# Kernel tuning notes

Measured on AMD Instinct MI355X. Metric: run time of the kernel, lower is better.

The kernel has to match this reference:

```python
import jax, jax.numpy as jnp
import numpy as np

B, N, C, H = 64, 577, 768, 12
D = C // H
SCALE = D ** -0.5


def setup_inputs() -> dict:
    key = jax.random.key(0)
    ks = jax.random.split(key, 5)
    s = 0.02
    return {
        "x": jax.random.normal(ks[0], (B, N, C), dtype=jnp.float32),
        "qkv_w": jax.random.normal(ks[1], (3 * C, C), dtype=jnp.float32) * s,
        "qkv_b": jax.random.normal(ks[2], (3 * C,), dtype=jnp.float32) * s,
        "proj_w": jax.random.normal(ks[3], (C, C), dtype=jnp.float32) * s,
        "proj_b": jax.random.normal(ks[4], (C,), dtype=jnp.float32) * s,
    }


def reference(x, qkv_w, qkv_b, proj_w, proj_b):
    b, n, c = x.shape
    # Full QKV projection (as in the original module): [B,N,3C] -> [B,N,3,H,D]
    qkv = (x @ qkv_w.T + qkv_b).reshape(b, n, 3, H, D)
    qc = qkv[:, :1, 0]   # class-token query only: [B,1,H,D]
    k = qkv[:, :, 1]     # [B,N,H,D]
    v = qkv[:, :, 2]     # [B,N,H,D]
    # single-query attention scores per head: [B,H,N]
    attn = jnp.einsum("bohd,bnhd->bhn", qc, k) * SCALE
    attn = jax.nn.softmax(attn, axis=-1)
    # weighted sum of values -> [B,H,D] -> [B,1,C]
    cls = jnp.einsum("bhn,bnhd->bhd", attn, v).reshape(b, 1, c)
    cls = cls @ proj_w.T + proj_b
    return jnp.concatenate([cls, x[:, 1:]], axis=1)
```

## Files before the change

kernel.cpp:

```cpp
#include <hip/hip_runtime.h>

#define Bz 64
#define Nn 577
#define Cc 768
#define Hh 12
#define Dd 64
#define SCALE 0.125f
#define YSEG 8

typedef __attribute__((ext_vector_type(8))) short short8;
typedef __attribute__((ext_vector_type(4))) float float4v;

__device__ __forceinline__ unsigned short bf16rne(float f) {
  unsigned u = __float_as_uint(f);
  u += 0x7FFFu + ((u >> 16) & 1u);
  return (unsigned short)(u >> 16);
}

__device__ __forceinline__ short8 cvt8(float4 a, float4 b) {
  short8 v;
  v[0] = (short)bf16rne(a.x); v[1] = (short)bf16rne(a.y);
  v[2] = (short)bf16rne(a.z); v[3] = (short)bf16rne(a.w);
  v[4] = (short)bf16rne(b.x); v[5] = (short)bf16rne(b.y);
  v[6] = (short)bf16rne(b.z); v[7] = (short)bf16rne(b.w);
  return v;
}

__device__ __forceinline__ short8 cvt8v(float4v a, float4v b) {
  short8 v;
  v[0] = (short)bf16rne(a[0]); v[1] = (short)bf16rne(a[1]);
  v[2] = (short)bf16rne(a[2]); v[3] = (short)bf16rne(a[3]);
  v[4] = (short)bf16rne(b[0]); v[5] = (short)bf16rne(b[1]);
  v[6] = (short)bf16rne(b[2]); v[7] = (short)bf16rne(b[3]);
  return v;
}


template <int MODE, int SEGS>
__global__ __launch_bounds__(256) void k_gemm64(const float* __restrict__ A,
                                                const float* __restrict__ W,
                                                const float* __restrict__ bias,
                                                float* __restrict__ out) {
  int tile = blockIdx.x;
  int jt = tile % 48, bt = tile / 48;
  int wave = threadIdx.x >> 6, lane = threadIdx.x & 63;
  int m = lane & 15, quad = lane >> 4;
  int brow = bt * 16 + m;
  int jrow = jt * 16 + m;
  size_t aoff;
  if (MODE == 0)      aoff = (size_t)brow * (Nn * Cc);
  else if (MODE == 1) aoff = (size_t)brow * (SEGS * Hh * Cc) + (size_t)(jt >> 2) * Cc;
  else                aoff = (size_t)brow * Cc;
  size_t woff = (MODE == 1) ? (size_t)(2 * Cc + jrow) * Cc : (size_t)jrow * Cc;
  const float4v* Ap = (const float4v*)(A + aoff) + wave * 48 + quad * 2;
  const float4v* Wp = (const float4v*)(W + woff) + wave * 48 + quad * 2;
  float4v acc = {0.f, 0.f, 0.f, 0.f};
#pragma unroll
  for (int s = 0; s < 6; ++s) {
    float4v a0, a1;
    if (MODE == 1 && SEGS > 1) {
      a0 = (float4v){0.f, 0.f, 0.f, 0.f};
      a1 = a0;
#pragma unroll
      for (int seg = 0; seg < SEGS; ++seg) {
        a0 += Ap[seg * 2304 + s * 8];
        a1 += Ap[seg * 2304 + s * 8 + 1];
      }
    } else {
      a0 = Ap[s * 8]; a1 = Ap[s * 8 + 1];
    }
    float4v w0 = Wp[s * 8], w1 = Wp[s * 8 + 1];
    acc = __builtin_amdgcn_mfma_f32_16x16x32_bf16(cvt8v(a0, a1), cvt8v(w0, w1),
                                                  acc, 0, 0, 0);
  }
  __shared__ float red[4][64][4];
#pragma unroll
  for (int reg = 0; reg < 4; ++reg) red[wave][lane][reg] = acc[reg];
  __syncthreads();
  if (wave == 0) {
#pragma unroll
    for (int reg = 0; reg < 4; ++reg) {
      float v = red[0][lane][reg] + red[1][lane][reg] +
                red[2][lane][reg] + red[3][lane][reg];
      int j = jt * 16 + m;
      int bb = bt * 16 + quad * 4 + reg;
      float bv = (MODE == 1) ? bias[2 * Cc + j] : bias[j];
      if (MODE == 2) out[(size_t)bb * (Nn * Cc) + j] = v + bv;
      else           out[(size_t)bb * Cc + j] = v + bv;
    }
  }
}

__global__ __launch_bounds__(256) void k_r(const float* __restrict__ qf,
                                           const float* __restrict__ qkv_w,
                                           unsigned short* __restrict__ rb) {
  int h = blockIdx.x % Hh, bg = blockIdx.x / Hh;
  int t = threadIdx.x;
  __shared__ float qs2[Dd][4];
  {
    int bb = t >> 6, d = t & 63;
    qs2[d][bb] = qf[(size_t)(bg * 4 + bb) * Cc + h * Dd + d];
  }
  __syncthreads();
  float acc[4][3];
#pragma unroll
  for (int bb = 0; bb < 4; ++bb)
#pragma unroll
    for (int i = 0; i < 3; ++i) acc[bb][i] = 0.f;
  const float* wk = qkv_w + (size_t)(Cc + h * Dd) * Cc;
  for (int d = 0; d < Dd; ++d) {
    float w0 = wk[(size_t)d * Cc + t];
    float w1 = wk[(size_t)d * Cc + t + 256];
    float w2 = wk[(size_t)d * Cc + t + 512];
    float4 qa = *(const float4*)&qs2[d][0];
    float qv[4] = {qa.x, qa.y, qa.z, qa.w};
#pragma unroll
    for (int bb = 0; bb < 4; ++bb) {
      acc[bb][0] += qv[bb] * w0;
      acc[bb][1] += qv[bb] * w1;
      acc[bb][2] += qv[bb] * w2;
    }
  }
#pragma unroll
  for (int bb = 0; bb < 4; ++bb) {
    size_t base = (size_t)(bg * 4 + bb) * 12288 + h * 8;
#pragma unroll
    for (int i = 0; i < 3; ++i) {
      int c = t + i * 256;
      int s = c >> 5, qq = (c >> 3) & 3, j = c & 7;
      rb[base + s * 512 + qq * 128 + j] = bf16rne(acc[bb][i] * SCALE);
    }
  }
}

__global__ __launch_bounds__(512) void k_logits(const float* __restrict__ x,
                                                const unsigned short* __restrict__ rb,
                                                float* __restrict__ logits) {
  int b = blockIdx.x / 10, tile = blockIdx.x % 10;
  int wave = threadIdx.x >> 6, lane = threadIdx.x & 63;
  int g = wave & 3, kh = wave >> 2;
  int m = lane & 15, quad = lane >> 4;
  int n = tile * 64 + g * 16 + m;
  int nc = n > 576 ? 576 : n;
  const short8* ag = (const short8*)(rb + (size_t)b * 12288);
  const float4* xg = (const float4*)(x + (size_t)b * Nn * Cc) + (size_t)nc * 192 + quad * 2;
  float4v acc = {0.f, 0.f, 0.f, 0.f};
#pragma unroll
  for (int i = 0; i < 12; ++i) {
    int s = kh * 12 + i;
    short8 a = ag[s * 64 + quad * 16 + m];
    float4 f0 = xg[s * 8], f1 = xg[s * 8 + 1];
    acc = __builtin_amdgcn_mfma_f32_16x16x32_bf16(a, cvt8(f0, f1), acc, 0, 0, 0);
  }
  __shared__ float red[4][64][4];
  if (kh == 1) {
#pragma unroll
    for (int reg = 0; reg < 4; ++reg) red[g][lane][reg] = acc[reg];
  }
  __syncthreads();
  if (kh == 0 && n < Nn) {
#pragma unroll
    for (int reg = 0; reg < 4; ++reg) {
      int hh = quad * 4 + reg;
      if (hh < Hh)
        logits[((size_t)b * Hh + hh) * Nn + n] = acc[reg] + red[g][lane][reg];
    }
  }
}

__global__ __launch_bounds__(64) void k_softmax(const float* __restrict__ logits,
                                                float* __restrict__ attnT) {
  int bh = blockIdx.x;
  int b = bh / Hh, h = bh % Hh;
  const float* row = logits + (size_t)bh * Nn;
  int t = threadIdx.x;
  float vals[10];
  float m = -1e30f;
#pragma unroll
  for (int i = 0; i < 10; ++i) {
    int n = i * 64 + t;
    vals[i] = (n < Nn) ? row[n] : -1e30f;
    m = fmaxf(m, vals[i]);
  }
#pragma unroll
  for (int off = 32; off; off >>= 1) m = fmaxf(m, __shfl_down(m, off));
  m = __shfl(m, 0);
  float s = 0.f;
#pragma unroll
  for (int i = 0; i < 10; ++i) { vals[i] = __expf(vals[i] - m); s += vals[i]; }
#pragma unroll
  for (int off = 32; off; off >>= 1) s += __shfl_down(s, off);
  float inv = 1.f / __shfl(s, 0);
#pragma unroll
  for (int i = 0; i < 10; ++i) {
    int n = i * 64 + t;
    if (n < Nn) attnT[((size_t)b * Nn + n) * Hh + h] = vals[i] * inv;
  }
}

__global__ __launch_bounds__(576) void k_y3c(const float* __restrict__ x,
                                             const float* __restrict__ attnT,
                                             float* __restrict__ ypart,
                                             float* __restrict__ out) {
  int b = blockIdx.x / YSEG, seg = blockIdx.x % YSEG;
  int c4 = threadIdx.x % 192;
  int sub = threadIdx.x / 192;
  int n0 = seg * Nn / YSEG, n1 = (seg + 1) * Nn / YSEG;
  int len = n1 - n0;
  int a0 = n0 + sub * len / 3, a1 = n0 + (sub + 1) * len / 3;
  float4v acc[Hh];
#pragma unroll
  for (int h = 0; h < Hh; ++h) acc[h] = (float4v){0.f, 0.f, 0.f, 0.f};
  const float4v* x4 = (const float4v*)(x + (size_t)b * Nn * Cc);
  float4v* o4 = (float4v*)(out + (size_t)b * Nn * Cc);
  const float* at = attnT + (size_t)b * Nn * Hh;
#pragma unroll 8
  for (int n = a0; n < a1; ++n) {
    float4v xv = x4[(size_t)n * 192 + c4];
    if (n)
      __builtin_nontemporal_store(xv, o4 + (size_t)n * 192 + c4);
#pragma unroll
    for (int h = 0; h < Hh; ++h) acc[h] += at[n * Hh + h] * xv;
  }
  __shared__ float4v red[192][Hh];
  if (sub == 2) {
#pragma unroll
    for (int h = 0; h < Hh; ++h) red[c4][h] = acc[h];
  }
  __syncthreads();
  if (sub == 1) {
#pragma unroll
    for (int h = 0; h < Hh; ++h) { acc[h] += red[c4][h]; red[c4][h] = acc[h]; }
  }
  __syncthreads();
  if (sub == 0) {
    float4v* yp = (float4v*)(ypart + ((size_t)(b * YSEG + seg)) * (Hh * Cc));
#pragma unroll
    for (int h = 0; h < Hh; ++h) yp[h * 192 + c4] = acc[h] + red[c4][h];
  }
}

__global__ __launch_bounds__(256) void k_zero(float* __restrict__ y) {
  ((float4*)y)[blockIdx.x * 256 + threadIdx.x] = make_float4(0.f, 0.f, 0.f, 0.f);
}

__global__ __launch_bounds__(192) void k_y_atomic(const float* __restrict__ x,
                                                  const float* __restrict__ attnT,
                                                  float* __restrict__ y) {
  int b = blockIdx.x / YSEG, seg = blockIdx.x % YSEG;
  int n0 = seg * Nn / YSEG, n1 = (seg + 1) * Nn / YSEG;
  int c4 = threadIdx.x;
  float4 acc[Hh];
#pragma unroll
  for (int h = 0; h < Hh; ++h) acc[h] = make_float4(0.f, 0.f, 0.f, 0.f);
  const float4* x4 = (const float4*)(x + (size_t)b * Nn * Cc);
  const float* at = attnT + (size_t)b * Nn * Hh;
#pragma unroll 8
  for (int n = n0; n < n1; ++n) {
    float4 xv = x4[(size_t)n * 192 + c4];
#pragma unroll
    for (int h = 0; h < Hh; ++h) {
      float a = at[n * Hh + h];
      acc[h].x += a * xv.x; acc[h].y += a * xv.y;
      acc[h].z += a * xv.z; acc[h].w += a * xv.w;
    }
  }
  float* yb = y + (size_t)b * Hh * Cc;
#pragma unroll
  for (int h = 0; h < Hh; ++h) {
    float* p = yb + h * Cc + c4 * 4;
    atomicAdd(p + 0, acc[h].x); atomicAdd(p + 1, acc[h].y);
    atomicAdd(p + 2, acc[h].z); atomicAdd(p + 3, acc[h].w);
  }
}

__global__ __launch_bounds__(256) void k_copy(const float* __restrict__ x,
                                              float* __restrict__ out) {
  int idx = blockIdx.x * 256 + threadIdx.x;
  const float4* xi = (const float4*)x;
  float4* oo = (float4*)out;
  for (int i = idx; i < 7077888; i += 262144) {
    int b = i / 110592;
    int r = i - b * 110592;
    size_t off = (size_t)b * 110784 + 192 + r;
    oo[off] = xi[off];
  }
}

extern "C" void kernel_launch(void* const* d_in, const int* in_sizes, int n_in,
                              void* d_out, int out_size, void* d_ws, size_t ws_size,
                              hipStream_t stream) {
  const float* x      = (const float*)d_in[0];
  const float* qkv_w  = (const float*)d_in[1];
  const float* qkv_b  = (const float*)d_in[2];
  const float* proj_w = (const float*)d_in[3];
  const float* proj_b = (const float*)d_in[4];
  float* out = (float*)d_out;
  float* ws = (float*)d_ws;

  unsigned short* rb = (unsigned short*)ws;
  float* qf     = ws + 393216;
  float* logits = ws + 442368;
  float* attnT  = ws + 885504;
  float* ypart  = ws + 1328640;
  float* cls    = ws + 6047232;

  const size_t NEED_PART = (size_t)6096384 * 4;

  if (ws_size >= NEED_PART) {
    k_gemm64<0, 1><<<192, 256, 0, stream>>>(x, qkv_w, qkv_b, qf);
    k_r<<<192, 256, 0, stream>>>(qf, qkv_w, rb);
    k_logits<<<Bz * 10, 512, 0, stream>>>(x, rb, logits);
    k_softmax<<<Bz * Hh, 64, 0, stream>>>(logits, attnT);
    k_y3c<<<Bz * YSEG, 576, 0, stream>>>(x, attnT, ypart, out);
    k_gemm64<1, YSEG><<<192, 256, 0, stream>>>(ypart, qkv_w, qkv_b, cls);
    k_gemm64<2, 1><<<192, 256, 0, stream>>>(cls, proj_w, proj_b, out);
  } else {
    float* y     = ws + 1328640;
    float* cls_c = ws + 1918464;
    k_zero<<<576, 256, 0, stream>>>(y);
    k_gemm64<0, 1><<<192, 256, 0, stream>>>(x, qkv_w, qkv_b, qf);
    k_r<<<192, 256, 0, stream>>>(qf, qkv_w, rb);
    k_logits<<<Bz * 10, 512, 0, stream>>>(x, rb, logits);
    k_softmax<<<Bz * Hh, 64, 0, stream>>>(logits, attnT);
    k_y_atomic<<<Bz * YSEG, 192, 0, stream>>>(x, attnT, y);
    k_gemm64<1, 1><<<192, 256, 0, stream>>>(y, qkv_w, qkv_b, cls_c);
    k_gemm64<2, 1><<<192, 256, 0, stream>>>(cls_c, proj_w, proj_b, out);
  }
}
```

Before: 292.7 us.

## Fuse q projection into k_r and softmax into value-weighted sum kernel

Computes the class-token query projection inside the k-folding kernel, removing the separate q GEMM launch and its workspace round trip. The logits kernel drops the split-K across waves and its shared-memory reduction, so each wave runs the full 24-step reduction. Softmax is folded into the y kernel: each block recomputes per-head max and sum from logits and applies exp on the fly, removing the softmax kernel and the attnT buffer. In exchange, max/sum work is repeated by every segment block and exp is evaluated inside the hot loop, and logits are read with a strided per-head pattern. The fallback path also gains a k_copy launch.

```diff
diff --git a/kernel.cpp b/kernel.cpp
--- a/kernel.cpp
+++ b/kernel.cpp
@@ -91,15 +91,32 @@
   }
 }
 
-__global__ __launch_bounds__(256) void k_r(const float* __restrict__ qf,
-                                           const float* __restrict__ qkv_w,
-                                           unsigned short* __restrict__ rb) {
+__global__ __launch_bounds__(256) void k_rq(const float* __restrict__ x,
+                                            const float* __restrict__ qkv_w,
+                                            const float* __restrict__ qkv_b,
+                                            unsigned short* __restrict__ rb) {
   int h = blockIdx.x % Hh, bg = blockIdx.x / Hh;
   int t = threadIdx.x;
+  __shared__ float x0s[4 * Cc];
   __shared__ float qs2[Dd][4];
   {
-    int bb = t >> 6, d = t & 63;
-    qs2[d][bb] = qf[(size_t)(bg * 4 + bb) * Cc + h * Dd + d];
+    const float4v* xg = (const float4v*)x;
+#pragma unroll
+    for (int k = 0; k < 3; ++k) {
+      int slot = t + k * 256;
+      int bb = slot / 192, c4 = slot % 192;
+      ((float4v*)x0s)[slot] = xg[(size_t)(bg * 4 + bb) * 110784 + c4];
+    }
+  }
+  __syncthreads();
+  {
+    int d = t & 63, bb = t >> 6;
+    const float4v* wrow = (const float4v*)(qkv_w + (size_t)(h * Dd + d) * Cc);
+    const float4v* xr = (const float4v*)x0s + bb * 192;
+    float4v a = {0.f, 0.f, 0.f, 0.f};
+#pragma unroll 4
+    for (int c = 0; c < 192; ++c) a += wrow[c] * xr[c];
+    qs2[d][bb] = a[0] + a[1] + a[2] + a[3] + qkv_b[h * Dd + d];
   }
   __syncthreads();
   float acc[4][3];
@@ -133,37 +150,28 @@
   }
 }
 
-__global__ __launch_bounds__(512) void k_logits(const float* __restrict__ x,
+__global__ __launch_bounds__(256) void k_logits(const float* __restrict__ x,
                                                 const unsigned short* __restrict__ rb,
                                                 float* __restrict__ logits) {
   int b = blockIdx.x / 10, tile = blockIdx.x % 10;
   int wave = threadIdx.x >> 6, lane = threadIdx.x & 63;
-  int g = wave & 3, kh = wave >> 2;
   int m = lane & 15, quad = lane >> 4;
-  int n = tile * 64 + g * 16 + m;
+  int n = tile * 64 + wave * 16 + m;
   int nc = n > 576 ? 576 : n;
   const short8* ag = (const short8*)(rb + (size_t)b * 12288);
   const float4* xg = (const float4*)(x + (size_t)b * Nn * Cc) + (size_t)nc * 192 + quad * 2;
   float4v acc = {0.f, 0.f, 0.f, 0.f};
-#pragma unroll
-  for (int i = 0; i < 12; ++i) {
-    int s = kh * 12 + i;
+#pragma unroll 8
+  for (int s = 0; s < 24; ++s) {
     short8 a = ag[s * 64 + quad * 16 + m];
     float4 f0 = xg[s * 8], f1 = xg[s * 8 + 1];
     acc = __builtin_amdgcn_mfma_f32_16x16x32_bf16(a, cvt8(f0, f1), acc, 0, 0, 0);
   }
-  __shared__ float red[4][64][4];
-  if (kh == 1) {
-#pragma unroll
-    for (int reg = 0; reg < 4; ++reg) red[g][lane][reg] = acc[reg];
-  }
-  __syncthreads();
-  if (kh == 0 && n < Nn) {
+  if (n < Nn) {
 #pragma unroll
     for (int reg = 0; reg < 4; ++reg) {
       int hh = quad * 4 + reg;
-      if (hh < Hh)
-        logits[((size_t)b * Hh + hh) * Nn + n] = acc[reg] + red[g][lane][reg];
+      if (hh < Hh) logits[((size_t)b * Hh + hh) * Nn + n] = acc[reg];
     }
   }
 }
@@ -198,13 +206,44 @@
   }
 }
 
-__global__ __launch_bounds__(576) void k_y3c(const float* __restrict__ x,
-                                             const float* __restrict__ attnT,
+__global__ __launch_bounds__(576) void k_y3s(const float* __restrict__ x,
+                                             const float* __restrict__ logits,
                                              float* __restrict__ ypart,
                                              float* __restrict__ out) {
   int b = blockIdx.x / YSEG, seg = blockIdx.x % YSEG;
   int c4 = threadIdx.x % 192;
   int sub = threadIdx.x / 192;
+  const float* lg = logits + (size_t)b * Hh * Nn;
+  __shared__ float red1[576];
+  __shared__ float sm_m[Hh], sm_inv[Hh];
+  {
+    int h = threadIdx.x / 48, j = threadIdx.x % 48;
+    float mx = -1e30f;
+    for (int n = j; n < Nn; n += 48) mx = fmaxf(mx, lg[h * Nn + n]);
+    red1[threadIdx.x] = mx;
+    __syncthreads();
+    if (j == 0) {
+      float mm = red1[h * 48];
+      for (int k = 1; k < 48; ++k) mm = fmaxf(mm, red1[h * 48 + k]);
+      sm_m[h] = mm;
+    }
+    __syncthreads();
+    float mh = sm_m[h];
+    float s = 0.f;
+    for (int n = j; n < Nn; n += 48) s += __expf(lg[h * Nn + n] - mh);
+    red1[threadIdx.x] = s;
+    __syncthreads();
+    if (j == 0) {
+      float l = 0.f;
+      for (int k = 0; k < 48; ++k) l += red1[h * 48 + k];
+      sm_inv[h] = 1.f / l;
+    }
+    __syncthreads();
+  }
+  float mh[Hh], ih[Hh];
+#pragma unroll
+  for (int h = 0; h < Hh; ++h) { mh[h] = sm_m[h]; ih[h] = sm_inv[h]; }
+
   int n0 = seg * Nn / YSEG, n1 = (seg + 1) * Nn / YSEG;
   int len = n1 - n0;
   int a0 = n0 + sub * len / 3, a1 = n0 + (sub + 1) * len / 3;
@@ -213,14 +252,16 @@
   for (int h = 0; h < Hh; ++h) acc[h] = (float4v){0.f, 0.f, 0.f, 0.f};
   const float4v* x4 = (const float4v*)(x + (size_t)b * Nn * Cc);
   float4v* o4 = (float4v*)(out + (size_t)b * Nn * Cc);
-  const float* at = attnT + (size_t)b * Nn * Hh;
-#pragma unroll 8
+#pragma unroll 4
   for (int n = a0; n < a1; ++n) {
     float4v xv = x4[(size_t)n * 192 + c4];
     if (n)
       __builtin_nontemporal_store(xv, o4 + (size_t)n * 192 + c4);
 #pragma unroll
-    for (int h = 0; h < Hh; ++h) acc[h] += at[n * Hh + h] * xv;
+    for (int h = 0; h < Hh; ++h) {
+      float a = __expf(lg[h * Nn + n] - mh[h]) * ih[h];
+      acc[h] += a * xv;
+    }
   }
   __shared__ float4v red[192][Hh];
   if (sub == 2) {
@@ -299,7 +340,6 @@
   float* ws = (float*)d_ws;
 
   unsigned short* rb = (unsigned short*)ws;
-  float* qf     = ws + 393216;
   float* logits = ws + 442368;
   float* attnT  = ws + 885504;
   float* ypart  = ws + 1328640;
@@ -308,23 +348,21 @@
   const size_t NEED_PART = (size_t)6096384 * 4;
 
   if (ws_size >= NEED_PART) {
-    k_gemm64<0, 1><<<192, 256, 0, stream>>>(x, qkv_w, qkv_b, qf);
-    k_r<<<192, 256, 0, stream>>>(qf, qkv_w, rb);
-    k_logits<<<Bz * 10, 512, 0, stream>>>(x, rb, logits);
-    k_softmax<<<Bz * Hh, 64, 0, stream>>>(logits, attnT);
-    k_y3c<<<Bz * YSEG, 576, 0, stream>>>(x, attnT, ypart, out);
+    k_rq<<<192, 256, 0, stream>>>(x, qkv_w, qkv_b, rb);
+    k_logits<<<Bz * 10, 256, 0, stream>>>(x, rb, logits);
+    k_y3s<<<Bz * YSEG, 576, 0, stream>>>(x, logits, ypart, out);
     k_gemm64<1, YSEG><<<192, 256, 0, stream>>>(ypart, qkv_w, qkv_b, cls);
     k_gemm64<2, 1><<<192, 256, 0, stream>>>(cls, proj_w, proj_b, out);
   } else {
     float* y     = ws + 1328640;
     float* cls_c = ws + 1918464;
     k_zero<<<576, 256, 0, stream>>>(y);
-    k_gemm64<0, 1><<<192, 256, 0, stream>>>(x, qkv_w, qkv_b, qf);
-    k_r<<<192, 256, 0, stream>>>(qf, qkv_w, rb);
-    k_logits<<<Bz * 10, 512, 0, stream>>>(x, rb, logits);
+    k_rq<<<192, 256, 0, stream>>>(x, qkv_w, qkv_b, rb);
+    k_logits<<<Bz * 10, 256, 0, stream>>>(x, rb, logits);
     k_softmax<<<Bz * Hh, 64, 0, stream>>>(logits, attnT);
     k_y_atomic<<<Bz * YSEG, 192, 0, stream>>>(x, attnT, y);
     k_gemm64<1, 1><<<192, 256, 0, stream>>>(y, qkv_w, qkv_b, cls_c);
     k_gemm64<2, 1><<<192, 256, 0, stream>>>(cls_c, proj_w, proj_b, out);
-  }
-}
+    k_copy<<<1024, 256, 0, stream>>>(x, out);
+  }
+}
```

After: 311.4 us. +6.4%, slower.
